# Kernel tuning notes

Hardware: AMD Instinct MI355X
Metric: run time of the kernel (lower is better)

The kernel has to match this reference:

```python
import jax, jax.numpy as jnp
import numpy as np

NUM_EXPERTS = 8
TOP_K = 2


def setup_inputs() -> dict:
    key = jax.random.key(0)
    ks = jax.random.split(key, 5)
    B, S, D, E, F = 4, 2048, 1024, NUM_EXPERTS, 4096
    x = jax.random.normal(ks[0], (B, S, D), dtype=jnp.float32)
    gate_w = jax.random.normal(ks[1], (E, D), dtype=jnp.float32) * 0.02
    W1 = jax.random.normal(ks[2], (E, D, F), dtype=jnp.float32) * 0.02
    W3 = jax.random.normal(ks[3], (E, D, F), dtype=jnp.float32) * 0.02
    W2 = jax.random.normal(ks[4], (E, F, D), dtype=jnp.float32) * 0.02
    return {"x": x, "gate_w": gate_w, "W1": W1, "W3": W3, "W2": W2}


def reference(x, gate_w, W1, W3, W2):
    B, S, D = x.shape
    E = gate_w.shape[0]
    xt = x.reshape(-1, D)                                   # [T, D], T = B*S
    T = xt.shape[0]
    router_logits = xt @ gate_w.T                           # [T, E]
    probs = jax.nn.softmax(router_logits.astype(jnp.float32), axis=-1)
    top_w, top_idx = jax.lax.top_k(probs, TOP_K)            # [T, k]
    top_w = top_w / jnp.sum(top_w, axis=-1, keepdims=True)  # renormalize top-k
    # dense per-(token, expert) combine weights; zero for non-selected experts
    dense_w = jnp.zeros((T, E), dtype=jnp.float32)
    dense_w = dense_w.at[jnp.arange(T)[:, None], top_idx].set(top_w)
    dense_w = dense_w.astype(x.dtype)
    out = jnp.zeros((T, D), dtype=x.dtype)
    for e in range(E):  # fixed small expert count; zero-weight tokens contribute 0
        h = jax.nn.silu(xt @ W1[e]) * (xt @ W3[e])          # [T, F]
        out = out + (h @ W2[e]) * dense_w[:, e:e + 1]
    return out.reshape(B, S, D), router_logits
```

## Files before the change

kernel.cpp:

```cpp
#include <hip/hip_runtime.h>
#include <hip/hip_bf16.h>
#include <stdint.h>

#define T_TOKENS 8192
#define D_DIM    1024
#define F_DIM    4096
#define NE       8
#define MAXTILES 136
#define PAIR_CAP 17408

typedef unsigned short u16;
typedef __attribute__((ext_vector_type(8))) __bf16 bf16x8;
typedef __attribute__((ext_vector_type(4))) float  f32x4;

__device__ __forceinline__ u16 f2bf(float f) {
    __hip_bfloat16 h = __float2bfloat16(f);
    return *reinterpret_cast<u16*>(&h);
}

__device__ __forceinline__ float bf2f(u16 r) {
    uint32_t u = ((uint32_t)r) << 16;
    return __uint_as_float(u);
}

__device__ __forceinline__ void gl_lds16(const void* g, void* l) {
    __builtin_amdgcn_global_load_lds(
        (const __attribute__((address_space(1))) uint32_t*)g,
        (__attribute__((address_space(3))) uint32_t*)l, 16, 0, 0);
}


__global__ __launch_bounds__(256) void k_router(
    const float* __restrict__ x, const float* __restrict__ gate_w,
    float* __restrict__ logits_out, int* __restrict__ ti,
    float* __restrict__ tw, int* __restrict__ ctrl)
{
    __shared__ float gw[NE * D_DIM];
    int tid = threadIdx.x;
    for (int i = tid; i < NE * D_DIM; i += 256) gw[i] = gate_w[i];
    __syncthreads();

    int wave = tid >> 6, lane = tid & 63;
    int t = blockIdx.x * 4 + wave;

    const float* xr = x + (size_t)t * D_DIM;
    float xv[16];
#pragma unroll
    for (int i = 0; i < 16; i++) xv[i] = xr[i * 64 + lane];

    float acc[NE];
#pragma unroll
    for (int e = 0; e < NE; e++) {
        float s = 0.f;
#pragma unroll
        for (int i = 0; i < 16; i++) s += xv[i] * gw[e * D_DIM + i * 64 + lane];
        for (int off = 32; off; off >>= 1) s += __shfl_down(s, off, 64);
        acc[e] = s;
    }

    if (lane == 0) {
#pragma unroll
        for (int e = 0; e < NE; e++) logits_out[t * NE + e] = acc[e];
        int i0 = 0; float v0 = acc[0];
        for (int e = 1; e < NE; e++) if (acc[e] > v0) { v0 = acc[e]; i0 = e; }
        int i1 = -1; float v1 = -3.0e38f;
        for (int e = 0; e < NE; e++) if (e != i0 && acc[e] > v1) { v1 = acc[e]; i1 = e; }
        float e1 = expf(v1 - v0);
        float s  = 1.f + e1;
        float w0 = 1.f / s, w1 = e1 / s;
        ti[t * 2 + 0] = i0; ti[t * 2 + 1] = i1;
        tw[t * 2 + 0] = w0; tw[t * 2 + 1] = w1;
        atomicAdd(&ctrl[i0], 1);
        atomicAdd(&ctrl[i1], 1);
    }
}

__global__ void k_plan(int* __restrict__ ctrl)
{
    if (threadIdx.x != 0 || blockIdx.x != 0) return;
    int* counts  = ctrl;
    int* off     = ctrl + 16;
    int* tile_e  = ctrl + 64;
    int* tile_m0 = ctrl + 256;
    int o = 0, nt = 0;
    for (int e = 0; e < NE; e++) {
        off[e] = o;
        int c = counts[e];
        int tcnt = (c + 127) >> 7;
        for (int j = 0; j < tcnt; j++) { tile_e[nt] = e; tile_m0[nt] = o + j * 128; nt++; }
        o += tcnt << 7;
    }
    off[NE] = o;
    ctrl[32] = nt;
}

__global__ __launch_bounds__(256) void k_scatter(
    const int* __restrict__ ti, const float* __restrict__ tw,
    int* __restrict__ ctrl, int* __restrict__ pair_token, float* __restrict__ pair_w)
{
    int t = blockIdx.x * 256 + threadIdx.x;
    if (t >= T_TOKENS) return;
    int* off    = ctrl + 16;
    int* cursor = ctrl + 8;
#pragma unroll
    for (int k = 0; k < 2; k++) {
        int e = ti[t * 2 + k];
        int slot = off[e] + atomicAdd(&cursor[e], 1);
        pair_token[slot] = t;
        pair_w[slot] = tw[t * 2 + k];
    }
}

__global__ __launch_bounds__(256) void k_cvt_x(
    const float* __restrict__ x, u16* __restrict__ xb)
{
    size_t i = ((size_t)blockIdx.x * 256 + threadIdx.x) * 4;
    float4 v = *(const float4*)(x + i);
    ushort4 o;
    o.x = f2bf(v.x); o.y = f2bf(v.y); o.z = f2bf(v.z); o.w = f2bf(v.w);
    *(ushort4*)(xb + i) = o;
}

__global__ __launch_bounds__(256) void k_transpose_cvt(
    const float* __restrict__ src, u16* __restrict__ dst, int R, int C)
{
    __shared__ float tile[32][33];
    size_t base = (size_t)blockIdx.z * R * C;
    src += base; dst += base;
    int c0 = blockIdx.x * 32, r0 = blockIdx.y * 32;
    int tx = threadIdx.x & 31, ty = threadIdx.x >> 5;
#pragma unroll
    for (int i = 0; i < 32; i += 8)
        tile[ty + i][tx] = src[(size_t)(r0 + ty + i) * C + c0 + tx];
    __syncthreads();
#pragma unroll
    for (int i = 0; i < 32; i += 8)
        dst[(size_t)(c0 + ty + i) * R + r0 + tx] = f2bf(tile[tx][ty + i]);
}

template<int MODE>
__global__ __launch_bounds__(256, 4) void k_gemm1x(
    const u16* __restrict__ xb, const u16* __restrict__ wt,
    u16* __restrict__ hbuf, const int* __restrict__ pair_token,
    const int* __restrict__ ctrl)
{
    int ntiles = ctrl[32];
    int tile = blockIdx.y;
    if (tile >= ntiles) return;
    int e  = ctrl[64 + tile];
    int m0 = ctrl[256 + tile];
    int n0 = blockIdx.x * 128;

    const u16* we = wt + (size_t)e * F_DIM * D_DIM;

    __shared__ __align__(16) u16 As[128 * 32];
    __shared__ __align__(16) u16 Bs[128 * 32];

    int tid  = threadIdx.x;
    int lane = tid & 63, wave = tid >> 6;

    int r_a = tid >> 2, kc = tid & 3;
    int tok0 = pair_token[m0 + r_a];
    int tok1 = pair_token[m0 + r_a + 64];
    const u16* gA0 = xb + (size_t)tok0 * D_DIM + kc * 8;
    const u16* gA1 = xb + (size_t)tok1 * D_DIM + kc * 8;
    const u16* gB0 = we + (size_t)(n0 + r_a) * D_DIM + kc * 8;
    const u16* gB1 = we + (size_t)(n0 + r_a + 64) * D_DIM + kc * 8;
    u16* lA0 = As + tid * 8;
    u16* lA1 = As + tid * 8 + 2048;
    u16* lB0 = Bs + tid * 8;
    u16* lB1 = Bs + tid * 8 + 2048;

    int wr = wave >> 1, wc = wave & 1;
    int quad = lane >> 4, mn = lane & 15;

    f32x4 acc[4][4] = {};

    for (int k0 = 0; k0 < D_DIM; k0 += 32) {
        gl_lds16(gA0 + k0, lA0);
        gl_lds16(gA1 + k0, lA1);
        gl_lds16(gB0 + k0, lB0);
        gl_lds16(gB1 + k0, lB1);
        __syncthreads();

        bf16x8 af[4], bf[4];
#pragma unroll
        for (int i = 0; i < 4; i++)
            af[i] = *(const bf16x8*)(As + (wr * 64 + i * 16 + mn) * 32 + quad * 8);
#pragma unroll
        for (int j = 0; j < 4; j++)
            bf[j] = *(const bf16x8*)(Bs + (wc * 64 + j * 16 + mn) * 32 + quad * 8);
#pragma unroll
        for (int i = 0; i < 4; i++)
#pragma unroll
            for (int j = 0; j < 4; j++)
                acc[i][j] = __builtin_amdgcn_mfma_f32_16x16x32_bf16(af[i], bf[j], acc[i][j], 0, 0, 0);
        __syncthreads();
    }

#pragma unroll
    for (int i = 0; i < 4; i++)
#pragma unroll
        for (int j = 0; j < 4; j++)
#pragma unroll
            for (int r = 0; r < 4; r++) {
                int row = wr * 64 + i * 16 + quad * 4 + r;
                int col = n0 + wc * 64 + j * 16 + mn;
                size_t idx = (size_t)(m0 + row) * F_DIM + col;
                float v = acc[i][j][r];
                if (MODE == 0) {
                    float s = v * (1.f / (1.f + __expf(-v)));
                    hbuf[idx] = f2bf(s);
                } else {
                    float s = bf2f(hbuf[idx]);
                    hbuf[idx] = f2bf(s * v);
                }
            }
}

__global__ __launch_bounds__(256, 4) void k_gemm2(
    const u16* __restrict__ h, const u16* __restrict__ w2t,
    float* __restrict__ out, const int* __restrict__ pair_token,
    const float* __restrict__ pair_w, const int* __restrict__ ctrl)
{
    int ntiles = ctrl[32];
    int tile = blockIdx.y;
    if (tile >= ntiles) return;
    int e  = ctrl[64 + tile];
    int m0 = ctrl[256 + tile];
    int n0 = blockIdx.x * 128;

    const u16* w2e = w2t + (size_t)e * D_DIM * F_DIM;

    __shared__ __align__(16) u16 As[128 * 32];
    __shared__ __align__(16) u16 Bs[128 * 32];

    int tid  = threadIdx.x;
    int lane = tid & 63, wave = tid >> 6;

    int r_a = tid >> 2, kc = tid & 3;
    const u16* gA0 = h   + (size_t)(m0 + r_a) * F_DIM + kc * 8;
    const u16* gA1 = h   + (size_t)(m0 + r_a + 64) * F_DIM + kc * 8;
    const u16* gB0 = w2e + (size_t)(n0 + r_a) * F_DIM + kc * 8;
    const u16* gB1 = w2e + (size_t)(n0 + r_a + 64) * F_DIM + kc * 8;
    u16* lA0 = As + tid * 8;
    u16* lA1 = As + tid * 8 + 2048;
    u16* lB0 = Bs + tid * 8;
    u16* lB1 = Bs + tid * 8 + 2048;

    int wr = wave >> 1, wc = wave & 1;
    int quad = lane >> 4, mn = lane & 15;

    f32x4 acc[4][4] = {};

    for (int k0 = 0; k0 < F_DIM; k0 += 32) {
        gl_lds16(gA0 + k0, lA0);
        gl_lds16(gA1 + k0, lA1);
        gl_lds16(gB0 + k0, lB0);
        gl_lds16(gB1 + k0, lB1);
        __syncthreads();

        bf16x8 af[4], bf[4];
#pragma unroll
        for (int i = 0; i < 4; i++)
            af[i] = *(const bf16x8*)(As + (wr * 64 + i * 16 + mn) * 32 + quad * 8);
#pragma unroll
        for (int j = 0; j < 4; j++)
            bf[j] = *(const bf16x8*)(Bs + (wc * 64 + j * 16 + mn) * 32 + quad * 8);
#pragma unroll
        for (int i = 0; i < 4; i++)
#pragma unroll
            for (int j = 0; j < 4; j++)
                acc[i][j] = __builtin_amdgcn_mfma_f32_16x16x32_bf16(af[i], bf[j], acc[i][j], 0, 0, 0);
        __syncthreads();
    }

#pragma unroll
    for (int i = 0; i < 4; i++)
#pragma unroll
        for (int r = 0; r < 4; r++) {
            int row = wr * 64 + i * 16 + quad * 4 + r;
            int prow = m0 + row;
            int tokv = pair_token[prow];
            float wv = pair_w[prow];
#pragma unroll
            for (int j = 0; j < 4; j++) {
                int col = n0 + wc * 64 + j * 16 + mn;
                atomicAdd(&out[(size_t)tokv * D_DIM + col], acc[i][j][r] * wv);
            }
        }
}

extern "C" void kernel_launch(void* const* d_in, const int* in_sizes, int n_in,
                              void* d_out, int out_size, void* d_ws, size_t ws_size,
                              hipStream_t stream)
{
    const float* x      = (const float*)d_in[0];
    const float* gate_w = (const float*)d_in[1];
    const float* W1     = (const float*)d_in[2];
    const float* W3     = (const float*)d_in[3];
    const float* W2     = (const float*)d_in[4];
    float* out = (float*)d_out;
    float* logits_out = out + (size_t)T_TOKENS * D_DIM;

    char* ws = (char*)d_ws;
    int*   ctrl       = (int*)ws;
    int*   pair_token = (int*)(ws + 4096);
    float* pair_w     = (float*)(ws + 4096 + 69632);
    int*   ti         = (int*)(ws + 143360);
    float* tw         = (float*)(ws + 208896);
    u16*   xb         = (u16*)(ws + 1048576);
    u16*   w1t        = (u16*)(ws + 17825792);
    u16*   w3t        = (u16*)(ws + 84934656);
    u16*   w2t        = (u16*)(ws + 152043520);
    u16*   h          = (u16*)(ws + 219152384);

    hipMemsetAsync(d_out, 0, (size_t)T_TOKENS * D_DIM * sizeof(float), stream);
    hipMemsetAsync(ws, 0, 143360, stream);

    k_router<<<T_TOKENS / 4, 256, 0, stream>>>(x, gate_w, logits_out, ti, tw, ctrl);
    k_plan<<<1, 64, 0, stream>>>(ctrl);
    k_scatter<<<T_TOKENS / 256, 256, 0, stream>>>(ti, tw, ctrl, pair_token, pair_w);

    k_cvt_x<<<(T_TOKENS * D_DIM) / (256 * 4), 256, 0, stream>>>(x, xb);
    dim3 tg1(128, 32, NE);
    k_transpose_cvt<<<tg1, 256, 0, stream>>>(W1, w1t, D_DIM, F_DIM);
    k_transpose_cvt<<<tg1, 256, 0, stream>>>(W3, w3t, D_DIM, F_DIM);
    dim3 tg2(32, 128, NE);
    k_transpose_cvt<<<tg2, 256, 0, stream>>>(W2, w2t, F_DIM, D_DIM);

    dim3 g1(F_DIM / 128, MAXTILES);
    k_gemm1x<0><<<g1, 256, 0, stream>>>(xb, w1t, h, pair_token, ctrl);
    k_gemm1x<1><<<g1, 256, 0, stream>>>(xb, w3t, h, pair_token, ctrl);
    dim3 g2(D_DIM / 128, MAXTILES);
    k_gemm2<<<g2, 256, 0, stream>>>(h, w2t, out, pair_token, pair_w, ctrl);
}
```

Measured before the change: 1.369 ms.

## Fuse W1/W3 GEMMs into one kernel, double-buffer LDS, remap blocks for XCD locality

Replaces the two separate gate/up GEMM launches with one 512-thread kernel. One half of the waves computes x@W1 and the other half x@W3 over a shared A tile, then the W3 results are exchanged through LDS so SiLU(a)*b is written once, avoiding the read-modify-write of h. Both GEMMs now double-buffer their LDS stages so the next k-slice loads while the current one computes. A block-index swizzle groups work across the 8 XCDs for better cache reuse. The cost is more LDS per block and lower occupancy.

```diff
diff --git a/kernel.cpp b/kernel.cpp
--- a/kernel.cpp
+++ b/kernel.cpp
@@ -7,7 +7,6 @@
 #define F_DIM    4096
 #define NE       8
 #define MAXTILES 136
-#define PAIR_CAP 17408
 
 typedef unsigned short u16;
 typedef __attribute__((ext_vector_type(8))) __bf16 bf16x8;
@@ -16,11 +15,6 @@
 __device__ __forceinline__ u16 f2bf(float f) {
     __hip_bfloat16 h = __float2bfloat16(f);
     return *reinterpret_cast<u16*>(&h);
-}
-
-__device__ __forceinline__ float bf2f(u16 r) {
-    uint32_t u = ((uint32_t)r) << 16;
-    return __uint_as_float(u);
 }
 
 __device__ __forceinline__ void gl_lds16(const void* g, void* l) {
@@ -138,84 +132,112 @@
         dst[(size_t)(c0 + ty + i) * R + r0 + tx] = f2bf(tile[tx][ty + i]);
 }
 
-template<int MODE>
-__global__ __launch_bounds__(256, 4) void k_gemm1x(
-    const u16* __restrict__ xb, const u16* __restrict__ wt,
-    u16* __restrict__ hbuf, const int* __restrict__ pair_token,
-    const int* __restrict__ ctrl)
+__global__ __launch_bounds__(512, 4) void k_gemm1f(
+    const u16* __restrict__ xb, const u16* __restrict__ w1t,
+    const u16* __restrict__ w3t, u16* __restrict__ hbuf,
+    const int* __restrict__ pair_token, const int* __restrict__ ctrl)
 {
     int ntiles = ctrl[32];
-    int tile = blockIdx.y;
+    const int nwg = 32 * MAXTILES;
+    int orig = blockIdx.x;
+    int w = (orig & 7) * (nwg >> 3) + (orig >> 3);
+    int tile = w % MAXTILES;
+    int nblk = w / MAXTILES;
     if (tile >= ntiles) return;
     int e  = ctrl[64 + tile];
     int m0 = ctrl[256 + tile];
-    int n0 = blockIdx.x * 128;
-
-    const u16* we = wt + (size_t)e * F_DIM * D_DIM;
-
-    __shared__ __align__(16) u16 As[128 * 32];
-    __shared__ __align__(16) u16 Bs[128 * 32];
+    int n0 = nblk * 128;
+
+    const u16* we1 = w1t + (size_t)e * F_DIM * D_DIM;
+    const u16* we3 = w3t + (size_t)e * F_DIM * D_DIM;
+
+    __shared__ __align__(16) char smem[49152];
+    u16* As  = (u16*)smem;
+    u16* B1s = (u16*)(smem + 16384);
+    u16* B3s = (u16*)(smem + 32768);
+    float* ex = (float*)smem;
 
     int tid  = threadIdx.x;
     int lane = tid & 63, wave = tid >> 6;
-
-    int r_a = tid >> 2, kc = tid & 3;
-    int tok0 = pair_token[m0 + r_a];
-    int tok1 = pair_token[m0 + r_a + 64];
-    const u16* gA0 = xb + (size_t)tok0 * D_DIM + kc * 8;
-    const u16* gA1 = xb + (size_t)tok1 * D_DIM + kc * 8;
-    const u16* gB0 = we + (size_t)(n0 + r_a) * D_DIM + kc * 8;
-    const u16* gB1 = we + (size_t)(n0 + r_a + 64) * D_DIM + kc * 8;
-    u16* lA0 = As + tid * 8;
-    u16* lA1 = As + tid * 8 + 2048;
-    u16* lB0 = Bs + tid * 8;
-    u16* lB1 = Bs + tid * 8 + 2048;
-
-    int wr = wave >> 1, wc = wave & 1;
+    int half = wave >> 2, w4 = wave & 3;
+    int wr = w4 >> 1, wc = w4 & 1;
     int quad = lane >> 4, mn = lane & 15;
 
+    int r_s = tid >> 2, kc = tid & 3;
+    int tok = pair_token[m0 + r_s];
+    const u16* gA  = xb  + (size_t)tok * D_DIM + kc * 8;
+    const u16* gB1 = we1 + (size_t)(n0 + r_s) * D_DIM + kc * 8;
+    const u16* gB3 = we3 + (size_t)(n0 + r_s) * D_DIM + kc * 8;
+    u16* lA  = As  + tid * 8;
+    u16* lB1 = B1s + tid * 8;
+    u16* lB3 = B3s + tid * 8;
+
+    const u16* Bsel = half ? B3s : B1s;
+
     f32x4 acc[4][4] = {};
 
-    for (int k0 = 0; k0 < D_DIM; k0 += 32) {
-        gl_lds16(gA0 + k0, lA0);
-        gl_lds16(gA1 + k0, lA1);
-        gl_lds16(gB0 + k0, lB0);
-        gl_lds16(gB1 + k0, lB1);
+    auto stage = [&](int buf, int k0) {
+        gl_lds16(gA  + k0, lA  + buf * 4096);
+        gl_lds16(gB1 + k0, lB1 + buf * 4096);
+        gl_lds16(gB3 + k0, lB3 + buf * 4096);
+    };
+    auto compute = [&](int buf) {
+        bf16x8 af[4], bfr[4];
+#pragma unroll
+        for (int i = 0; i < 4; i++)
+            af[i] = *(const bf16x8*)(As + buf * 4096 + (wr * 64 + i * 16 + mn) * 32 + quad * 8);
+#pragma unroll
+        for (int j = 0; j < 4; j++)
+            bfr[j] = *(const bf16x8*)(Bsel + buf * 4096 + (wc * 64 + j * 16 + mn) * 32 + quad * 8);
+#pragma unroll
+        for (int i = 0; i < 4; i++)
+#pragma unroll
+            for (int j = 0; j < 4; j++)
+                acc[i][j] = __builtin_amdgcn_mfma_f32_16x16x32_bf16(af[i], bfr[j], acc[i][j], 0, 0, 0);
+    };
+
+    stage(0, 0);
+    __syncthreads();
+    int cur = 0;
+    for (int k0 = 32; k0 < D_DIM; k0 += 32) {
+        stage(cur ^ 1, k0);
+        compute(cur);
         __syncthreads();
-
-        bf16x8 af[4], bf[4];
-#pragma unroll
-        for (int i = 0; i < 4; i++)
-            af[i] = *(const bf16x8*)(As + (wr * 64 + i * 16 + mn) * 32 + quad * 8);
-#pragma unroll
-        for (int j = 0; j < 4; j++)
-            bf[j] = *(const bf16x8*)(Bs + (wc * 64 + j * 16 + mn) * 32 + quad * 8);
-#pragma unroll
-        for (int i = 0; i < 4; i++)
-#pragma unroll
-            for (int j = 0; j < 4; j++)
-                acc[i][j] = __builtin_amdgcn_mfma_f32_16x16x32_bf16(af[i], bf[j], acc[i][j], 0, 0, 0);
+        cur ^= 1;
+    }
+    compute(cur);
+    __syncthreads();
+
+    for (int round = 0; round < 2; round++) {
+        if (half == 1 && wr == round) {
+            float* exb = ex + (w4 & 1) * 4096;
+#pragma unroll
+            for (int i = 0; i < 4; i++)
+#pragma unroll
+                for (int j = 0; j < 4; j++)
+#pragma unroll
+                    for (int r = 0; r < 4; r++)
+                        exb[(i * 16 + quad * 4 + r) * 64 + j * 16 + mn] = acc[i][j][r];
+        }
         __syncthreads();
-    }
-
-#pragma unroll
-    for (int i = 0; i < 4; i++)
-#pragma unroll
-        for (int j = 0; j < 4; j++)
-#pragma unroll
-            for (int r = 0; r < 4; r++) {
-                int row = wr * 64 + i * 16 + quad * 4 + r;
-                int col = n0 + wc * 64 + j * 16 + mn;
-                size_t idx = (size_t)(m0 + row) * F_DIM + col;
-                float v = acc[i][j][r];
-                if (MODE == 0) {
-                    float s = v * (1.f / (1.f + __expf(-v)));
-                    hbuf[idx] = f2bf(s);
-                } else {
-                    float s = bf2f(hbuf[idx]);
-                    hbuf[idx] = f2bf(s * v);
-                }
-            }
+        if (half == 0 && wr == round) {
+            const float* exb = ex + (w4 & 1) * 4096;
+#pragma unroll
+            for (int i = 0; i < 4; i++)
+#pragma unroll
+                for (int j = 0; j < 4; j++)
+#pragma unroll
+                    for (int r = 0; r < 4; r++) {
+                        float v1 = acc[i][j][r];
+                        float v3 = exb[(i * 16 + quad * 4 + r) * 64 + j * 16 + mn];
+                        float sl = v1 * (1.f / (1.f + __expf(-v1)));
+                        size_t idx = (size_t)(m0 + wr * 64 + i * 16 + quad * 4 + r) * F_DIM
+                                   + n0 + wc * 64 + j * 16 + mn;
+                        hbuf[idx] = f2bf(sl * v3);
+                    }
+        }
+        __syncthreads();
+    }
 }
 
 __global__ __launch_bounds__(256, 4) void k_gemm2(
@@ -224,16 +246,20 @@
     const float* __restrict__ pair_w, const int* __restrict__ ctrl)
 {
     int ntiles = ctrl[32];
-    int tile = blockIdx.y;
+    const int nwg = 8 * MAXTILES;
+    int orig = blockIdx.x;
+    int w = (orig & 7) * (nwg >> 3) + (orig >> 3);
+    int tile = w % MAXTILES;
+    int nblk = w / MAXTILES;
     if (tile >= ntiles) return;
     int e  = ctrl[64 + tile];
     int m0 = ctrl[256 + tile];
-    int n0 = blockIdx.x * 128;
+    int n0 = nblk * 128;
 
     const u16* w2e = w2t + (size_t)e * D_DIM * F_DIM;
 
-    __shared__ __align__(16) u16 As[128 * 32];
-    __shared__ __align__(16) u16 Bs[128 * 32];
+    __shared__ __align__(16) u16 As[2][4096];
+    __shared__ __align__(16) u16 Bs[2][4096];
 
     int tid  = threadIdx.x;
     int lane = tid & 63, wave = tid >> 6;
@@ -243,37 +269,43 @@
     const u16* gA1 = h   + (size_t)(m0 + r_a + 64) * F_DIM + kc * 8;
     const u16* gB0 = w2e + (size_t)(n0 + r_a) * F_DIM + kc * 8;
     const u16* gB1 = w2e + (size_t)(n0 + r_a + 64) * F_DIM + kc * 8;
-    u16* lA0 = As + tid * 8;
-    u16* lA1 = As + tid * 8 + 2048;
-    u16* lB0 = Bs + tid * 8;
-    u16* lB1 = Bs + tid * 8 + 2048;
 
     int wr = wave >> 1, wc = wave & 1;
     int quad = lane >> 4, mn = lane & 15;
 
     f32x4 acc[4][4] = {};
 
-    for (int k0 = 0; k0 < F_DIM; k0 += 32) {
-        gl_lds16(gA0 + k0, lA0);
-        gl_lds16(gA1 + k0, lA1);
-        gl_lds16(gB0 + k0, lB0);
-        gl_lds16(gB1 + k0, lB1);
+    auto stage = [&](int buf, int k0) {
+        gl_lds16(gA0 + k0, &As[buf][tid * 8]);
+        gl_lds16(gA1 + k0, &As[buf][tid * 8 + 2048]);
+        gl_lds16(gB0 + k0, &Bs[buf][tid * 8]);
+        gl_lds16(gB1 + k0, &Bs[buf][tid * 8 + 2048]);
+    };
+    auto compute = [&](int buf) {
+        bf16x8 af[4], bfr[4];
+#pragma unroll
+        for (int i = 0; i < 4; i++)
+            af[i] = *(const bf16x8*)(&As[buf][(wr * 64 + i * 16 + mn) * 32 + quad * 8]);
+#pragma unroll
+        for (int j = 0; j < 4; j++)
+            bfr[j] = *(const bf16x8*)(&Bs[buf][(wc * 64 + j * 16 + mn) * 32 + quad * 8]);
+#pragma unroll
+        for (int i = 0; i < 4; i++)
+#pragma unroll
+            for (int j = 0; j < 4; j++)
+                acc[i][j] = __builtin_amdgcn_mfma_f32_16x16x32_bf16(af[i], bfr[j], acc[i][j], 0, 0, 0);
+    };
+
+    stage(0, 0);
+    __syncthreads();
+    int cur = 0;
+    for (int k0 = 32; k0 < F_DIM; k0 += 32) {
+        stage(cur ^ 1, k0);
+        compute(cur);
         __syncthreads();
-
-        bf16x8 af[4], bf[4];
-#pragma unroll
-        for (int i = 0; i < 4; i++)
-            af[i] = *(const bf16x8*)(As + (wr * 64 + i * 16 + mn) * 32 + quad * 8);
-#pragma unroll
-        for (int j = 0; j < 4; j++)
-            bf[j] = *(const bf16x8*)(Bs + (wc * 64 + j * 16 + mn) * 32 + quad * 8);
-#pragma unroll
-        for (int i = 0; i < 4; i++)
-#pragma unroll
-            for (int j = 0; j < 4; j++)
-                acc[i][j] = __builtin_amdgcn_mfma_f32_16x16x32_bf16(af[i], bf[j], acc[i][j], 0, 0, 0);
-        __syncthreads();
-    }
+        cur ^= 1;
+    }
+    compute(cur);
 
 #pragma unroll
     for (int i = 0; i < 4; i++)
@@ -329,9 +361,6 @@
     dim3 tg2(32, 128, NE);
     k_transpose_cvt<<<tg2, 256, 0, stream>>>(W2, w2t, F_DIM, D_DIM);
 
-    dim3 g1(F_DIM / 128, MAXTILES);
-    k_gemm1x<0><<<g1, 256, 0, stream>>>(xb, w1t, h, pair_token, ctrl);
-    k_gemm1x<1><<<g1, 256, 0, stream>>>(xb, w3t, h, pair_token, ctrl);
-    dim3 g2(D_DIM / 128, MAXTILES);
-    k_gemm2<<<g2, 256, 0, stream>>>(h, w2t, out, pair_token, pair_w, ctrl);
-}
+    k_gemm1f<<<32 * MAXTILES, 512, 0, stream>>>(xb, w1t, w3t, h, pair_token, ctrl);
+    k_gemm2<<<8 * MAXTILES, 256, 0, stream>>>(h, w2t, out, pair_token, pair_w, ctrl);
+}
```

Measured after the change: 1.589 ms. 1.16x slower.
